# Optimization experiments

Measured on AMD Instinct MI355X. Metric: run time of the kernel, lower is better.

Reference implementation:

```python
import jax, jax.numpy as jnp
import numpy as np


def c2p_gather(feat, ind):
    # feat: [B, C, M] cell features; ind: [B, N, 2] (slot 0 = cell index)
    B, C, _ = feat.shape
    idx = ind[:, :, 0]                                   # [B, N]
    idx3 = jnp.broadcast_to(idx[:, None, :], (B, C, idx.shape[1]))
    return jnp.take_along_axis(feat, idx3, axis=2)       # [B, C, N]


def p2c_scatter(x, ind, num_cells):
    # x: [B, C, Nn] point features; ind: [B, Nn, 2]; scatter-add into [B, C, M]
    idx = ind[:, :, 0]                                   # [B, Nn]

    def per_batch(xb, ib):
        # xb: [C, Nn] -> segment_sum over points -> [M, C]
        return jax.ops.segment_sum(xb.T, ib, num_segments=num_cells).T

    return jax.vmap(per_batch)(x, idx)                   # [B, C, M]


def setup_inputs() -> dict:
    key = jax.random.key(0)
    ks = jax.random.split(key, 8)
    B, Cv, Cr, E, Co = 2, 64, 20, 64, 64
    Mv, Mr = 100000, 50000
    N = 262144            # gathered points; os=8 -> bundle=4 -> Nn=65536 nodes
    Nn = N // 4
    return {
        "v_feat": jax.random.normal(ks[0], (B, Cv, Mv), jnp.float32),
        "r_feat": jax.random.normal(ks[1], (B, Cr, Mr), jnp.float32),
        "Wq": jax.random.normal(ks[2], (E, Cr), jnp.float32) * 0.1,
        "Wk": jax.random.normal(ks[3], (E, Cv), jnp.float32) * 0.1,
        "Wv": jax.random.normal(ks[4], (E, Cv), jnp.float32) * 0.1,
        "Wo": jax.random.normal(ks[5], (Co, E), jnp.float32) * 0.1,
        "v2p_ind": jax.random.randint(ks[6], (B, N, 2), 0, Mv).astype(jnp.int64),
        "r2p_ind": jax.random.randint(ks[7], (B, Nn, 2), 0, Mr).astype(jnp.int64),
        "os": 8,
    }


def reference(v_feat, r_feat, Wq, Wk, Wv, Wo, v2p_ind, r2p_ind, os):
    bundle = max(1, int(os) // 2)
    B, Cv, _ = v_feat.shape
    Mr = r_feat.shape[2]

    # c2p gather of detached features (module calls .detach())
    v_pp = c2p_gather(jax.lax.stop_gradient(v_feat), v2p_ind)       # [B, Cv, N]
    N = v_pp.shape[2]
    Nn = N // bundle
    v_nodes = v_pp.reshape(B, Cv, Nn, bundle)                        # bundle splits
    r_pp = c2p_gather(jax.lax.stop_gradient(r_feat), r2p_ind)        # [B, Cr, Nn]

    # attent1d: query from r feature, keys/values from the neighbor bundle
    E = Wq.shape[0]
    q = jnp.einsum("ec,bcn->ben", Wq, r_pp)                          # [B, E, Nn]
    k = jnp.einsum("ec,bcnm->benm", Wk, v_nodes)                     # [B, E, Nn, bundle]
    v = jnp.einsum("ec,bcnm->benm", Wv, v_nodes)
    scores = jnp.einsum("ben,benm->bnm", q, k) / jnp.sqrt(jnp.float32(E))
    attn = jax.nn.softmax(scores, axis=-1)                           # over bundle
    agg = jnp.einsum("bnm,benm->ben", attn, v)                       # [B, E, Nn]
    xr = jnp.einsum("oe,ben->bon", Wo, agg)                          # [B, Co, Nn]

    # p2c scatter back to r-cell layout (size taken from r_feat)
    xr_mapped = p2c_scatter(xr, r2p_ind, Mr)                         # [B, Co, Mr]
    return xr_mapped
```

## Files before the change

kernel.cpp:

```cpp
#include <hip/hip_runtime.h>
#include <cstdint>

#define BB 2
#define CV 64
#define CR 20
#define EE 64
#define CO 64
#define NZ 256
#define TM 128

__global__ __launch_bounds__(256) void k_setup(
    const float* __restrict__ vf, const float* __restrict__ Wq,
    const float* __restrict__ Wk, const float* __restrict__ Wv,
    const float* __restrict__ Wo, const int* __restrict__ r2p,
    float* __restrict__ vt, float* __restrict__ G, float* __restrict__ H,
    int* __restrict__ flag, float4* __restrict__ xs4,
    int Mv, int ntm, int NT, int xsE4) {
  int bid = blockIdx.x, t = threadIdx.x;
  if (bid < NT) {
    __shared__ float tile[64 * 128];
    int b = bid / ntm, tm = bid % ntm;
    int m0 = tm * TM;
    const float* src = vf + (size_t)b * CV * Mv;
    float* dst = vt + (size_t)b * Mv * 64;
    if (((Mv & 3) == 0) && (m0 + TM <= Mv)) {
      #pragma unroll
      for (int p = 0; p < 8; ++p) {
        int c = p * 8 + (t >> 5), mq = t & 31;
        float4 v = *(const float4*)&src[(size_t)c * Mv + m0 + 4 * mq];
        *(float4*)&tile[c * 128 + ((mq ^ (c & 31)) << 2)] = v;
      }
      __syncthreads();
      #pragma unroll
      for (int p = 0; p < 8; ++p) {
        int ml = p * 16 + (t >> 4), cq = t & 15;
        int mc = ml >> 2, mr = ml & 3;
        float4 w;
        w.x = tile[(4 * cq + 0) * 128 + ((mc ^ ((4 * cq + 0) & 31)) << 2) + mr];
        w.y = tile[(4 * cq + 1) * 128 + ((mc ^ ((4 * cq + 1) & 31)) << 2) + mr];
        w.z = tile[(4 * cq + 2) * 128 + ((mc ^ ((4 * cq + 2) & 31)) << 2) + mr];
        w.w = tile[(4 * cq + 3) * 128 + ((mc ^ ((4 * cq + 3) & 31)) << 2) + mr];
        *(float4*)&dst[(size_t)(m0 + ml) * 64 + 4 * cq] = w;
      }
    } else {
      for (int p = 0; p < 32; ++p) {
        int idx = p * 256 + t;
        int c = idx >> 7, ml = idx & 127;
        int m = m0 + ml;
        float v = (m < Mv) ? src[(size_t)c * Mv + m] : 0.f;
        tile[c * 128 + (((ml >> 2) ^ (c & 31)) << 2) + (ml & 3)] = v;
      }
      __syncthreads();
      for (int p = 0; p < 32; ++p) {
        int idx = p * 256 + t;
        int ml = idx >> 6, c = idx & 63;
        int m = m0 + ml;
        if (m < Mv)
          dst[(size_t)m * 64 + c] =
              tile[c * 128 + (((ml >> 2) ^ (c & 31)) << 2) + (ml & 3)];
      }
    }
    return;
  }
  int r = bid - NT;
  if (r < 5) {
    int idx = r * 256 + t;
    if (idx < CR * CV) {
      int cr = idx / CV, cv = idx % CV;
      float s = 0.f;
      #pragma unroll
      for (int e = 0; e < EE; ++e) s += Wq[e * CR + cr] * Wk[e * CV + cv];
      G[idx] = s;
    }
  } else if (r < 21) {
    int idx = (r - 5) * 256 + t;
    int o = idx >> 6, c = idx & 63;
    float s = 0.f;
    #pragma unroll
    for (int e = 0; e < EE; ++e) s += Wo[o * EE + e] * Wv[e * CV + c];
    H[idx] = s;
  } else if (r == 21) {
    __shared__ int any;
    if (t == 0) any = 0;
    __syncthreads();
    int nz = 0;
    for (int i = t; i < 4096; i += 256) nz |= r2p[2 * i + 1];
    if (nz) atomicOr(&any, 1);
    __syncthreads();
    if (t == 0) *flag = (any == 0) ? 4 : 2;
  } else {
    int z = r - 22;
    float4 zz = make_float4(0.f, 0.f, 0.f, 0.f);
    for (int i = z * 256 + t; i < xsE4; i += NZ * 256) xs4[i] = zz;
  }
}

__global__ __launch_bounds__(256) void k_gq(
    const float* __restrict__ rf, const float* __restrict__ G,
    float* __restrict__ gq, int Mr, int ntj) {
  __shared__ float Gl[CR * 64];
  __shared__ float rt[CR][68];
  int b = blockIdx.x / ntj, tj = blockIdx.x % ntj;
  int j0 = tj * 64;
  int t = threadIdx.x;
  for (int idx = t; idx < CR * 64; idx += 256) Gl[idx] = G[idx];
  const float* src = rf + (size_t)b * CR * Mr;
  for (int idx = t; idx < CR * 64; idx += 256) {
    int c = idx >> 6, jl = idx & 63;
    int j = j0 + jl;
    rt[c][jl] = (j < Mr) ? src[(size_t)c * Mr + j] : 0.f;
  }
  __syncthreads();
  int ti = t & 15, tjq = t >> 4;
  float acc[4][4];
  #pragma unroll
  for (int a = 0; a < 4; ++a)
    #pragma unroll
    for (int q = 0; q < 4; ++q) acc[a][q] = 0.f;
  for (int c = 0; c < CR; ++c) {
    float4 gx = *(const float4*)&Gl[c * 64 + 4 * ti];
    float4 xj = *(const float4*)&rt[c][4 * tjq];
    #pragma unroll
    for (int a = 0; a < 4; ++a) {
      float xv = (a == 0) ? xj.x : (a == 1) ? xj.y : (a == 2) ? xj.z : xj.w;
      acc[a][0] += xv * gx.x;
      acc[a][1] += xv * gx.y;
      acc[a][2] += xv * gx.z;
      acc[a][3] += xv * gx.w;
    }
  }
  #pragma unroll
  for (int a = 0; a < 4; ++a) {
    int j = j0 + 4 * tjq + a;
    if (j < Mr) {
      float4 w = make_float4(acc[a][0], acc[a][1], acc[a][2], acc[a][3]);
      *(float4*)&gq[((size_t)b * Mr + j) * 64 + 4 * ti] = w;
    }
  }
}

template <int WS>
__device__ __forceinline__ void load_idx(
    const int* __restrict__ r2p, const int* __restrict__ v2p,
    int p, int Nn, int N, int P,
    int& b, int& j, int& i0, int& i1, int& i2, int& i3) {
  if (p >= P) { b = 0; j = 0; i0 = i1 = i2 = i3 = 0; return; }
  b = (p >= Nn) ? 1 : 0;
  int n = p - b * Nn;
  j = r2p[((size_t)b * Nn + n) * WS];
  const int* vi = v2p + ((size_t)b * N + (size_t)n * 4) * WS;
  if (WS == 2) {
    int4 w0 = *(const int4*)vi;
    int4 w1 = *(const int4*)(vi + 4);
    i0 = w0.x; i1 = w0.z; i2 = w1.x; i3 = w1.z;
  } else {
    i0 = vi[0]; i1 = vi[1 * WS]; i2 = vi[2 * WS]; i3 = vi[3 * WS];
  }
}

__device__ __forceinline__ float gred16(float h) {
  h += __shfl_xor(h, 1);
  h += __shfl_xor(h, 2);
  h += __shfl_xor(h, 4);
  h += __shfl_xor(h, 8);
  return h;
}

template <int WS>
__device__ __forceinline__ void main_loop(
    const float* __restrict__ vt, const float* __restrict__ gq,
    const int* __restrict__ v2p, const int* __restrict__ r2p,
    float* __restrict__ xs, float* __restrict__ my,
    int Mv, int Mr, int N, int Nn, int P, int gw, int totWaves) {
  int t = threadIdx.x;
  int lane = t & 63, sl = t & 15, grp = (t >> 4) & 3;
  int stride = totWaves * 4;
  int base = gw * 4;
  if (base >= P) return;
  int b, j, i0, i1, i2, i3;
  load_idx<WS>(r2p, v2p, base + grp, Nn, N, P, b, j, i0, i1, i2, i3);
  while (true) {
    const float* gqb = gq + (size_t)b * Mr * 64;
    const float* vb  = vt + (size_t)b * Mv * 64;
    float4 q4 = *(const float4*)&gqb[(size_t)j  * 64 + 4 * sl];
    float4 c0 = *(const float4*)&vb [(size_t)i0 * 64 + 4 * sl];
    float4 c1 = *(const float4*)&vb [(size_t)i1 * 64 + 4 * sl];
    float4 c2 = *(const float4*)&vb [(size_t)i2 * 64 + 4 * sl];
    float4 c3 = *(const float4*)&vb [(size_t)i3 * 64 + 4 * sl];
    int nb = base + stride;
    int b2 = 0, j2 = 0, p0 = 0, p1 = 0, p2 = 0, p3 = 0;
    bool more = nb < P;
    if (more)
      load_idx<WS>(r2p, v2p, nb + grp, Nn, N, P, b2, j2, p0, p1, p2, p3);
    float s0 = gred16(q4.x * c0.x + q4.y * c0.y + q4.z * c0.z + q4.w * c0.w);
    float s1 = gred16(q4.x * c1.x + q4.y * c1.y + q4.z * c1.z + q4.w * c1.w);
    float s2 = gred16(q4.x * c2.x + q4.y * c2.y + q4.z * c2.z + q4.w * c2.w);
    float s3 = gred16(q4.x * c3.x + q4.y * c3.y + q4.z * c3.z + q4.w * c3.w);
    s0 *= 0.125f; s1 *= 0.125f; s2 *= 0.125f; s3 *= 0.125f;
    float mx = fmaxf(fmaxf(s0, s1), fmaxf(s2, s3));
    float e0 = __expf(s0 - mx), e1 = __expf(s1 - mx);
    float e2 = __expf(s2 - mx), e3 = __expf(s3 - mx);
    float inv = 1.f / (e0 + e1 + e2 + e3);
    e0 *= inv; e1 *= inv; e2 *= inv; e3 *= inv;
    float4 ag;
    ag.x = e0 * c0.x + e1 * c1.x + e2 * c2.x + e3 * c3.x;
    ag.y = e0 * c0.y + e1 * c1.y + e2 * c2.y + e3 * c3.y;
    ag.z = e0 * c0.z + e1 * c1.z + e2 * c2.z + e3 * c3.z;
    ag.w = e0 * c0.w + e1 * c1.w + e2 * c2.w + e3 * c3.w;
    *(float4*)&my[grp * 68 + 4 * sl] = ag;
    #pragma unroll
    for (int g = 0; g < 4; ++g) {
      if (base + g < P) {
        int jg = __shfl(j, g * 16);
        int bg = ((base + g) >= Nn) ? 1 : 0;
        float v = my[g * 68 + lane];
        atomicAdd(&xs[((size_t)bg * Mr + jg) * 64 + lane], v);
      }
    }
    if (!more) break;
    base = nb; b = b2; j = j2; i0 = p0; i1 = p1; i2 = p2; i3 = p3;
  }
}

__global__ __launch_bounds__(256) void k_main(
    const float* __restrict__ vt, const float* __restrict__ gq,
    const int* __restrict__ v2p, const int* __restrict__ r2p,
    float* __restrict__ xs, const int* __restrict__ flag,
    int Mv, int Mr, int N, int Nn, int P, int totWaves) {
  __shared__ float sc[4 * 272];
  int wid = threadIdx.x >> 6;
  float* my = sc + wid * 272;
  int gw = blockIdx.x * 4 + wid;
  if (*flag == 2)
    main_loop<2>(vt, gq, v2p, r2p, xs, my, Mv, Mr, N, Nn, P, gw, totWaves);
  else
    main_loop<4>(vt, gq, v2p, r2p, xs, my, Mv, Mr, N, Nn, P, gw, totWaves);
}

__device__ __forceinline__ int hsw(int fidx) {
  return fidx ^ (((fidx >> 8) & 7) << 2);
}

__global__ __launch_bounds__(256) void k_out_t(
    const float* __restrict__ xs, const float* __restrict__ H,
    float* __restrict__ out, int Mr, int ntj) {
  __shared__ float Hl[CO * CV];
  __shared__ float xt[64][68];
  int b = blockIdx.x / ntj, tj = blockIdx.x % ntj;
  int j0 = tj * 64;
  int t = threadIdx.x;
  for (int idx = t; idx < CO * CV; idx += 256) Hl[hsw(idx)] = H[idx];
  const float* src = xs + (size_t)b * Mr * 64;
  #pragma unroll
  for (int k = 0; k < 4; ++k) {
    int jl = k * 16 + (t >> 4), c4 = t & 15;
    int j = j0 + jl;
    float4 v = (j < Mr) ? *(const float4*)&src[(size_t)j * 64 + 4 * c4]
                        : make_float4(0.f, 0.f, 0.f, 0.f);
    *(float4*)&xt[jl][4 * c4] = v;
  }
  __syncthreads();
  int ti = t & 15;
  int tjq4 = t >> 4;
  float acc[4][4];
  #pragma unroll
  for (int a = 0; a < 4; ++a)
    #pragma unroll
    for (int q = 0; q < 4; ++q) acc[a][q] = 0.f;
  #pragma unroll 4
  for (int cq = 0; cq < 16; ++cq) {
    float4 xv[4], hb[4];
    #pragma unroll
    for (int a = 0; a < 4; ++a)
      xv[a] = *(const float4*)&xt[4 * tjq4 + a][4 * cq];
    #pragma unroll
    for (int q = 0; q < 4; ++q) {
      int row = 4 * ti + q;
      hb[q] = *(const float4*)&Hl[hsw(row * 64 + 4 * cq)];
    }
    #pragma unroll
    for (int a = 0; a < 4; ++a)
      #pragma unroll
      for (int q = 0; q < 4; ++q)
        acc[a][q] += xv[a].x * hb[q].x + xv[a].y * hb[q].y +
                     xv[a].z * hb[q].z + xv[a].w * hb[q].w;
  }
  __syncthreads();
  #pragma unroll
  for (int a = 0; a < 4; ++a)
    #pragma unroll
    for (int q = 0; q < 4; ++q)
      xt[4 * ti + q][4 * tjq4 + a] = acc[a][q];
  __syncthreads();
  float* dst = out + (size_t)b * CO * Mr;
  #pragma unroll
  for (int k = 0; k < 4; ++k) {
    int o = k * 16 + (t >> 4), j4 = t & 15;
    int j = j0 + 4 * j4;
    if (j + 3 < Mr) {
      *(float4*)&dst[(size_t)o * Mr + j] = *(const float4*)&xt[o][4 * j4];
    } else {
      #pragma unroll
      for (int i = 0; i < 4; ++i)
        if (j + i < Mr) dst[(size_t)o * Mr + j + i] = xt[o][4 * j4 + i];
    }
  }
}

extern "C" void kernel_launch(void* const* d_in, const int* in_sizes, int n_in,
                              void* d_out, int out_size, void* d_ws, size_t ws_size,
                              hipStream_t stream) {
  const float* v_feat = (const float*)d_in[0];
  const float* r_feat = (const float*)d_in[1];
  const float* Wq = (const float*)d_in[2];
  const float* Wk = (const float*)d_in[3];
  const float* Wv = (const float*)d_in[4];
  const float* Wo = (const float*)d_in[5];
  const int* v2p = (const int*)d_in[6];
  const int* r2p = (const int*)d_in[7];

  int Mv = in_sizes[0] / (BB * CV);
  int Mr = in_sizes[1] / (BB * CR);
  int N  = in_sizes[6] / (BB * 2);
  int Nn = in_sizes[7] / (BB * 2);

  float* ws = (float*)d_ws;
  float* vt = ws;
  float* gq = vt + (size_t)BB * Mv * 64;
  float* xs = gq + (size_t)BB * Mr * 64;
  float* G  = xs + (size_t)BB * Mr * 64;
  float* H  = G + CR * CV;
  int* flag = (int*)(H + CO * CV);
  float* out = (float*)d_out;

  int ntm = (Mv + TM - 1) / TM;
  int NT = BB * ntm;
  int xsE4 = (BB * Mr * 64) / 4;
  k_setup<<<NT + 22 + NZ, 256, 0, stream>>>(v_feat, Wq, Wk, Wv, Wo, r2p,
                                            vt, G, H, flag, (float4*)xs,
                                            Mv, ntm, NT, xsE4);

  int ntj = (Mr + 63) / 64;
  k_gq<<<BB * ntj, 256, 0, stream>>>(r_feat, G, gq, Mr, ntj);

  int P = BB * Nn;
  int blocks = 2048;
  k_main<<<blocks, 256, 0, stream>>>(vt, gq, v2p, r2p, xs, flag,
                                     Mv, Mr, N, Nn, P, blocks * 4);

  k_out_t<<<BB * ntj, 256, 0, stream>>>(xs, H, out, Mr, ntj);
}
```

Baseline: 212.8 us.

## Fuse gq projection into setup kernel and flatten main loop to two nodes per wave

The separate k_gq launch is folded into k_setup: each gq block recomputes the small Wq^T·Wk matrix G in shared memory and then projects its r-feature tile, which removes one kernel launch and the G round-trip through global memory. The persistent grid-stride main loop is replaced by a one-shot grid in which each wave handles eight nodes as two independent batches, so ten gathers are issued together for more memory-level parallelism, with launch bounds raised to target higher occupancy. In exchange, every gq block redundantly recomputes G, and the software prefetch of the next iteration's indices is dropped.

```diff
diff --git a/kernel.cpp b/kernel.cpp
--- a/kernel.cpp
+++ b/kernel.cpp
@@ -10,15 +10,17 @@
 #define TM 128
 
 __global__ __launch_bounds__(256) void k_setup(
-    const float* __restrict__ vf, const float* __restrict__ Wq,
-    const float* __restrict__ Wk, const float* __restrict__ Wv,
-    const float* __restrict__ Wo, const int* __restrict__ r2p,
-    float* __restrict__ vt, float* __restrict__ G, float* __restrict__ H,
+    const float* __restrict__ vf, const float* __restrict__ rf,
+    const float* __restrict__ Wq, const float* __restrict__ Wk,
+    const float* __restrict__ Wv, const float* __restrict__ Wo,
+    const int* __restrict__ r2p,
+    float* __restrict__ vt, float* __restrict__ gq, float* __restrict__ H,
     int* __restrict__ flag, float4* __restrict__ xs4,
-    int Mv, int ntm, int NT, int xsE4) {
+    int Mv, int Mr, int ntm, int ntj, int NT, int NGQ, int xsE4) {
+  __shared__ float smem[64 * 128];
   int bid = blockIdx.x, t = threadIdx.x;
   if (bid < NT) {
-    __shared__ float tile[64 * 128];
+    float* tile = smem;
     int b = bid / ntm, tm = bid % ntm;
     int m0 = tm * TM;
     const float* src = vf + (size_t)b * CV * Mv;
@@ -63,23 +65,62 @@
     return;
   }
   int r = bid - NT;
-  if (r < 5) {
+  if (r < NGQ) {
+    float* Gl = smem;
+    float* rt = smem + 1280;
+    for (int idx = t; idx < CR * CV; idx += 256) {
+      int cr = idx / CV, cv = idx - cr * CV;
+      float s = 0.f;
+      #pragma unroll
+      for (int e = 0; e < EE; ++e) s += Wq[e * CR + cr] * Wk[e * CV + cv];
+      Gl[idx] = s;
+    }
+    int b = r / ntj, tj = r - b * ntj;
+    int j0 = tj * 64;
+    const float* src = rf + (size_t)b * CR * Mr;
+    for (int idx = t; idx < CR * 64; idx += 256) {
+      int c = idx >> 6, jl = idx & 63;
+      int j = j0 + jl;
+      rt[c * 68 + jl] = (j < Mr) ? src[(size_t)c * Mr + j] : 0.f;
+    }
+    __syncthreads();
+    int ti = t & 15, tjq = t >> 4;
+    float acc[4][4];
+    #pragma unroll
+    for (int a = 0; a < 4; ++a)
+      #pragma unroll
+      for (int q = 0; q < 4; ++q) acc[a][q] = 0.f;
+    for (int c = 0; c < CR; ++c) {
+      float4 gx = *(const float4*)&Gl[c * 64 + 4 * ti];
+      float4 xj = *(const float4*)&rt[c * 68 + 4 * tjq];
+      #pragma unroll
+      for (int a = 0; a < 4; ++a) {
+        float xv = (a == 0) ? xj.x : (a == 1) ? xj.y : (a == 2) ? xj.z : xj.w;
+        acc[a][0] += xv * gx.x;
+        acc[a][1] += xv * gx.y;
+        acc[a][2] += xv * gx.z;
+        acc[a][3] += xv * gx.w;
+      }
+    }
+    #pragma unroll
+    for (int a = 0; a < 4; ++a) {
+      int j = j0 + 4 * tjq + a;
+      if (j < Mr) {
+        float4 w = make_float4(acc[a][0], acc[a][1], acc[a][2], acc[a][3]);
+        *(float4*)&gq[((size_t)b * Mr + j) * 64 + 4 * ti] = w;
+      }
+    }
+    return;
+  }
+  r -= NGQ;
+  if (r < 16) {
     int idx = r * 256 + t;
-    if (idx < CR * CV) {
-      int cr = idx / CV, cv = idx % CV;
-      float s = 0.f;
-      #pragma unroll
-      for (int e = 0; e < EE; ++e) s += Wq[e * CR + cr] * Wk[e * CV + cv];
-      G[idx] = s;
-    }
-  } else if (r < 21) {
-    int idx = (r - 5) * 256 + t;
     int o = idx >> 6, c = idx & 63;
     float s = 0.f;
     #pragma unroll
     for (int e = 0; e < EE; ++e) s += Wo[o * EE + e] * Wv[e * CV + c];
     H[idx] = s;
-  } else if (r == 21) {
+  } else if (r == 16) {
     __shared__ int any;
     if (t == 0) any = 0;
     __syncthreads();
@@ -89,53 +130,9 @@
     __syncthreads();
     if (t == 0) *flag = (any == 0) ? 4 : 2;
   } else {
-    int z = r - 22;
+    int z = r - 17;
     float4 zz = make_float4(0.f, 0.f, 0.f, 0.f);
     for (int i = z * 256 + t; i < xsE4; i += NZ * 256) xs4[i] = zz;
-  }
-}
-
-__global__ __launch_bounds__(256) void k_gq(
-    const float* __restrict__ rf, const float* __restrict__ G,
-    float* __restrict__ gq, int Mr, int ntj) {
-  __shared__ float Gl[CR * 64];
-  __shared__ float rt[CR][68];
-  int b = blockIdx.x / ntj, tj = blockIdx.x % ntj;
-  int j0 = tj * 64;
-  int t = threadIdx.x;
-  for (int idx = t; idx < CR * 64; idx += 256) Gl[idx] = G[idx];
-  const float* src = rf + (size_t)b * CR * Mr;
-  for (int idx = t; idx < CR * 64; idx += 256) {
-    int c = idx >> 6, jl = idx & 63;
-    int j = j0 + jl;
-    rt[c][jl] = (j < Mr) ? src[(size_t)c * Mr + j] : 0.f;
-  }
-  __syncthreads();
-  int ti = t & 15, tjq = t >> 4;
-  float acc[4][4];
-  #pragma unroll
-  for (int a = 0; a < 4; ++a)
-    #pragma unroll
-    for (int q = 0; q < 4; ++q) acc[a][q] = 0.f;
-  for (int c = 0; c < CR; ++c) {
-    float4 gx = *(const float4*)&Gl[c * 64 + 4 * ti];
-    float4 xj = *(const float4*)&rt[c][4 * tjq];
-    #pragma unroll
-    for (int a = 0; a < 4; ++a) {
-      float xv = (a == 0) ? xj.x : (a == 1) ? xj.y : (a == 2) ? xj.z : xj.w;
-      acc[a][0] += xv * gx.x;
-      acc[a][1] += xv * gx.y;
-      acc[a][2] += xv * gx.z;
-      acc[a][3] += xv * gx.w;
-    }
-  }
-  #pragma unroll
-  for (int a = 0; a < 4; ++a) {
-    int j = j0 + 4 * tjq + a;
-    if (j < Mr) {
-      float4 w = make_float4(acc[a][0], acc[a][1], acc[a][2], acc[a][3]);
-      *(float4*)&gq[((size_t)b * Mr + j) * 64 + 4 * ti] = w;
-    }
   }
 }
 
@@ -166,75 +163,80 @@
   return h;
 }
 
+__device__ __forceinline__ float4 att4(float4 q4, float4 c0, float4 c1,
+                                       float4 c2, float4 c3) {
+  float s0 = gred16(q4.x * c0.x + q4.y * c0.y + q4.z * c0.z + q4.w * c0.w);
+  float s1 = gred16(q4.x * c1.x + q4.y * c1.y + q4.z * c1.z + q4.w * c1.w);
+  float s2 = gred16(q4.x * c2.x + q4.y * c2.y + q4.z * c2.z + q4.w * c2.w);
+  float s3 = gred16(q4.x * c3.x + q4.y * c3.y + q4.z * c3.z + q4.w * c3.w);
+  s0 *= 0.125f; s1 *= 0.125f; s2 *= 0.125f; s3 *= 0.125f;
+  float mx = fmaxf(fmaxf(s0, s1), fmaxf(s2, s3));
+  float e0 = __expf(s0 - mx), e1 = __expf(s1 - mx);
+  float e2 = __expf(s2 - mx), e3 = __expf(s3 - mx);
+  float inv = 1.f / (e0 + e1 + e2 + e3);
+  e0 *= inv; e1 *= inv; e2 *= inv; e3 *= inv;
+  float4 ag;
+  ag.x = e0 * c0.x + e1 * c1.x + e2 * c2.x + e3 * c3.x;
+  ag.y = e0 * c0.y + e1 * c1.y + e2 * c2.y + e3 * c3.y;
+  ag.z = e0 * c0.z + e1 * c1.z + e2 * c2.z + e3 * c3.z;
+  ag.w = e0 * c0.w + e1 * c1.w + e2 * c2.w + e3 * c3.w;
+  return ag;
+}
+
 template <int WS>
-__device__ __forceinline__ void main_loop(
+__device__ __forceinline__ void main_body(
     const float* __restrict__ vt, const float* __restrict__ gq,
     const int* __restrict__ v2p, const int* __restrict__ r2p,
     float* __restrict__ xs, float* __restrict__ my,
-    int Mv, int Mr, int N, int Nn, int P, int gw, int totWaves) {
+    int Mv, int Mr, int N, int Nn, int P) {
   int t = threadIdx.x;
   int lane = t & 63, sl = t & 15, grp = (t >> 4) & 3;
-  int stride = totWaves * 4;
-  int base = gw * 4;
+  int base = (blockIdx.x * 4 + (t >> 6)) * 8;
   if (base >= P) return;
-  int b, j, i0, i1, i2, i3;
-  load_idx<WS>(r2p, v2p, base + grp, Nn, N, P, b, j, i0, i1, i2, i3);
-  while (true) {
-    const float* gqb = gq + (size_t)b * Mr * 64;
-    const float* vb  = vt + (size_t)b * Mv * 64;
-    float4 q4 = *(const float4*)&gqb[(size_t)j  * 64 + 4 * sl];
-    float4 c0 = *(const float4*)&vb [(size_t)i0 * 64 + 4 * sl];
-    float4 c1 = *(const float4*)&vb [(size_t)i1 * 64 + 4 * sl];
-    float4 c2 = *(const float4*)&vb [(size_t)i2 * 64 + 4 * sl];
-    float4 c3 = *(const float4*)&vb [(size_t)i3 * 64 + 4 * sl];
-    int nb = base + stride;
-    int b2 = 0, j2 = 0, p0 = 0, p1 = 0, p2 = 0, p3 = 0;
-    bool more = nb < P;
-    if (more)
-      load_idx<WS>(r2p, v2p, nb + grp, Nn, N, P, b2, j2, p0, p1, p2, p3);
-    float s0 = gred16(q4.x * c0.x + q4.y * c0.y + q4.z * c0.z + q4.w * c0.w);
-    float s1 = gred16(q4.x * c1.x + q4.y * c1.y + q4.z * c1.z + q4.w * c1.w);
-    float s2 = gred16(q4.x * c2.x + q4.y * c2.y + q4.z * c2.z + q4.w * c2.w);
-    float s3 = gred16(q4.x * c3.x + q4.y * c3.y + q4.z * c3.z + q4.w * c3.w);
-    s0 *= 0.125f; s1 *= 0.125f; s2 *= 0.125f; s3 *= 0.125f;
-    float mx = fmaxf(fmaxf(s0, s1), fmaxf(s2, s3));
-    float e0 = __expf(s0 - mx), e1 = __expf(s1 - mx);
-    float e2 = __expf(s2 - mx), e3 = __expf(s3 - mx);
-    float inv = 1.f / (e0 + e1 + e2 + e3);
-    e0 *= inv; e1 *= inv; e2 *= inv; e3 *= inv;
-    float4 ag;
-    ag.x = e0 * c0.x + e1 * c1.x + e2 * c2.x + e3 * c3.x;
-    ag.y = e0 * c0.y + e1 * c1.y + e2 * c2.y + e3 * c3.y;
-    ag.z = e0 * c0.z + e1 * c1.z + e2 * c2.z + e3 * c3.z;
-    ag.w = e0 * c0.w + e1 * c1.w + e2 * c2.w + e3 * c3.w;
-    *(float4*)&my[grp * 68 + 4 * sl] = ag;
-    #pragma unroll
-    for (int g = 0; g < 4; ++g) {
-      if (base + g < P) {
-        int jg = __shfl(j, g * 16);
-        int bg = ((base + g) >= Nn) ? 1 : 0;
-        float v = my[g * 68 + lane];
-        atomicAdd(&xs[((size_t)bg * Mr + jg) * 64 + lane], v);
-      }
-    }
-    if (!more) break;
-    base = nb; b = b2; j = j2; i0 = p0; i1 = p1; i2 = p2; i3 = p3;
-  }
-}
-
-__global__ __launch_bounds__(256) void k_main(
+  int pA = base + grp, pB = base + grp + 4;
+  int bA, jA, a0, a1, a2, a3, bB, jB, b0, b1, b2, b3;
+  load_idx<WS>(r2p, v2p, pA, Nn, N, P, bA, jA, a0, a1, a2, a3);
+  load_idx<WS>(r2p, v2p, pB, Nn, N, P, bB, jB, b0, b1, b2, b3);
+  const float* gqA = gq + (size_t)bA * Mr * 64;
+  const float* vbA = vt + (size_t)bA * Mv * 64;
+  const float* gqB = gq + (size_t)bB * Mr * 64;
+  const float* vbB = vt + (size_t)bB * Mv * 64;
+  float4 qA  = *(const float4*)&gqA[(size_t)jA * 64 + 4 * sl];
+  float4 cA0 = *(const float4*)&vbA[(size_t)a0 * 64 + 4 * sl];
+  float4 cA1 = *(const float4*)&vbA[(size_t)a1 * 64 + 4 * sl];
+  float4 cA2 = *(const float4*)&vbA[(size_t)a2 * 64 + 4 * sl];
+  float4 cA3 = *(const float4*)&vbA[(size_t)a3 * 64 + 4 * sl];
+  float4 qB  = *(const float4*)&gqB[(size_t)jB * 64 + 4 * sl];
+  float4 cB0 = *(const float4*)&vbB[(size_t)b0 * 64 + 4 * sl];
+  float4 cB1 = *(const float4*)&vbB[(size_t)b1 * 64 + 4 * sl];
+  float4 cB2 = *(const float4*)&vbB[(size_t)b2 * 64 + 4 * sl];
+  float4 cB3 = *(const float4*)&vbB[(size_t)b3 * 64 + 4 * sl];
+  float4 agA = att4(qA, cA0, cA1, cA2, cA3);
+  *(float4*)&my[grp * 68 + 4 * sl] = agA;
+  float4 agB = att4(qB, cB0, cB1, cB2, cB3);
+  *(float4*)&my[(grp + 4) * 68 + 4 * sl] = agB;
+  #pragma unroll
+  for (int g = 0; g < 8; ++g) {
+    if (base + g < P) {
+      int jg = __shfl((g < 4) ? jA : jB, (g & 3) * 16);
+      int bg = ((base + g) >= Nn) ? 1 : 0;
+      float v = my[g * 68 + lane];
+      atomicAdd(&xs[((size_t)bg * Mr + jg) * 64 + lane], v);
+    }
+  }
+}
+
+__global__ __launch_bounds__(256, 8) void k_main(
     const float* __restrict__ vt, const float* __restrict__ gq,
     const int* __restrict__ v2p, const int* __restrict__ r2p,
     float* __restrict__ xs, const int* __restrict__ flag,
-    int Mv, int Mr, int N, int Nn, int P, int totWaves) {
-  __shared__ float sc[4 * 272];
-  int wid = threadIdx.x >> 6;
-  float* my = sc + wid * 272;
-  int gw = blockIdx.x * 4 + wid;
+    int Mv, int Mr, int N, int Nn, int P) {
+  __shared__ float sc[4 * 8 * 68];
+  float* my = sc + (threadIdx.x >> 6) * (8 * 68);
   if (*flag == 2)
-    main_loop<2>(vt, gq, v2p, r2p, xs, my, Mv, Mr, N, Nn, P, gw, totWaves);
+    main_body<2>(vt, gq, v2p, r2p, xs, my, Mv, Mr, N, Nn, P);
   else
-    main_loop<4>(vt, gq, v2p, r2p, xs, my, Mv, Mr, N, Nn, P, gw, totWaves);
+    main_body<4>(vt, gq, v2p, r2p, xs, my, Mv, Mr, N, Nn, P);
 }
 
 __device__ __forceinline__ int hsw(int fidx) {
@@ -328,25 +330,23 @@
   float* vt = ws;
   float* gq = vt + (size_t)BB * Mv * 64;
   float* xs = gq + (size_t)BB * Mr * 64;
-  float* G  = xs + (size_t)BB * Mr * 64;
-  float* H  = G + CR * CV;
+  float* H  = xs + (size_t)BB * Mr * 64;
   int* flag = (int*)(H + CO * CV);
   float* out = (float*)d_out;
 
   int ntm = (Mv + TM - 1) / TM;
+  int ntj = (Mr + 63) / 64;
   int NT = BB * ntm;
+  int NGQ = BB * ntj;
   int xsE4 = (BB * Mr * 64) / 4;
-  k_setup<<<NT + 22 + NZ, 256, 0, stream>>>(v_feat, Wq, Wk, Wv, Wo, r2p,
-                                            vt, G, H, flag, (float4*)xs,
-                                            Mv, ntm, NT, xsE4);
-
-  int ntj = (Mr + 63) / 64;
-  k_gq<<<BB * ntj, 256, 0, stream>>>(r_feat, G, gq, Mr, ntj);
+  k_setup<<<NT + NGQ + 17 + NZ, 256, 0, stream>>>(
+      v_feat, r_feat, Wq, Wk, Wv, Wo, r2p, vt, gq, H, flag, (float4*)xs,
+      Mv, Mr, ntm, ntj, NT, NGQ, xsE4);
 
   int P = BB * Nn;
-  int blocks = 2048;
+  int blocks = (P + 31) / 32;
   k_main<<<blocks, 256, 0, stream>>>(vt, gq, v2p, r2p, xs, flag,
-                                     Mv, Mr, N, Nn, P, blocks * 4);
+                                     Mv, Mr, N, Nn, P);
 
   k_out_t<<<BB * ntj, 256, 0, stream>>>(xs, H, out, Mr, ntj);
 }
```

Measured after the change: 210.4 us. About the same (-1.1%).
